# Kernel tuning notes

Measured on AMD Instinct MI355X. Metric: run time of the kernel, lower is better.

## Reference

```python
import jax, jax.numpy as jnp
import numpy as np

N_SRC = 100000
N_DST = 50000
N_EDGES = 1600000
D_IN = 128
D_OUT = 64


def setup_inputs() -> dict:
    key = jax.random.key(0)
    ks = jax.random.split(key, 6)
    x = jax.random.normal(ks[0], (N_SRC, D_IN), dtype=jnp.float32)
    W_l = jax.random.normal(ks[1], (D_IN, D_OUT), dtype=jnp.float32) * (1.0 / np.sqrt(D_IN))
    b_l = jax.random.normal(ks[2], (D_OUT,), dtype=jnp.float32) * 0.01
    W_r = jax.random.normal(ks[3], (D_IN, D_OUT), dtype=jnp.float32) * (1.0 / np.sqrt(D_IN))
    src = jax.random.randint(ks[4], (N_EDGES,), 0, N_SRC, dtype=jnp.int64)
    dst = jax.random.randint(ks[5], (N_EDGES,), 0, N_DST, dtype=jnp.int64)
    edge_index = jnp.stack([src, dst], axis=0)
    return {"x": x, "W_l": W_l, "b_l": b_l, "W_r": W_r,
            "edge_index": edge_index, "n_dst": N_DST}


def reference(x, W_l, b_l, W_r, edge_index, n_dst):
    src, dst = edge_index[0], edge_index[1]
    # gather source features along edges: [E, D_in]
    msgs = x[src]
    # mean aggregation at destination nodes
    agg = jax.ops.segment_sum(msgs, dst, num_segments=n_dst)          # [n_dst, D_in]
    cnt = jax.ops.segment_sum(jnp.ones_like(dst, dtype=x.dtype), dst,
                              num_segments=n_dst)                     # [n_dst]
    mean = agg / jnp.maximum(cnt, 1.0)[:, None]
    x_target = x[:n_dst]
    # SAGEConv: lin_l(mean_agg) + lin_r(x_target)
    out = mean @ W_l + b_l + x_target @ W_r                           # [n_dst, D_out]
    return jax.nn.log_softmax(out, axis=-1)
```

## Files before the change

### kernel.cpp

```cpp
#include <hip/hip_runtime.h>
#include <math.h>

#define DIN  128
#define DOUT 64
#define SLOT 96

__device__ inline unsigned short f2bf(float f) {
    unsigned u = __float_as_uint(f);
    u += 0x7fffu + ((u >> 16) & 1u);
    return (unsigned short)(u >> 16);
}
__device__ inline float bflo(unsigned u) { return __uint_as_float(u << 16); }
__device__ inline float bfhi(unsigned u) { return __uint_as_float(u & 0xffff0000u); }

__global__ void __launch_bounds__(256) build_k(
    const int* __restrict__ ei, unsigned* __restrict__ cnt,
    int* __restrict__ slots,
    const float* __restrict__ x, const float* __restrict__ Wl,
    const float* __restrict__ bl, const float* __restrict__ Wr,
    unsigned short* __restrict__ y, float* __restrict__ zout,
    int E, int nFill, int P, int nyb, int n_src, int n_dst, int cstr)
{
    __shared__ float s_x[16][DIN];
    const int b = blockIdx.x;
    const int fq = b / P;
    const bool isFill = ((b % P) == 0) && (fq < nFill);

    if (isFill) {
        int t = fq * 256 + threadIdx.x;
        int base = t * 8;
        if (base >= E) return;
        if (base + 8 <= E) {
            int4 sa = *(const int4*)(ei + base);
            int4 sb4 = *(const int4*)(ei + base + 4);
            int4 da = *(const int4*)(ei + E + base);
            int4 db = *(const int4*)(ei + E + base + 4);
            unsigned p0 = atomicAdd(&cnt[(size_t)da.x * cstr], 1u);
            unsigned p1 = atomicAdd(&cnt[(size_t)da.y * cstr], 1u);
            unsigned p2 = atomicAdd(&cnt[(size_t)da.z * cstr], 1u);
            unsigned p3 = atomicAdd(&cnt[(size_t)da.w * cstr], 1u);
            unsigned p4 = atomicAdd(&cnt[(size_t)db.x * cstr], 1u);
            unsigned p5 = atomicAdd(&cnt[(size_t)db.y * cstr], 1u);
            unsigned p6 = atomicAdd(&cnt[(size_t)db.z * cstr], 1u);
            unsigned p7 = atomicAdd(&cnt[(size_t)db.w * cstr], 1u);
            if (p0 < SLOT) slots[(size_t)da.x * SLOT + p0] = sa.x;
            if (p1 < SLOT) slots[(size_t)da.y * SLOT + p1] = sa.y;
            if (p2 < SLOT) slots[(size_t)da.z * SLOT + p2] = sa.z;
            if (p3 < SLOT) slots[(size_t)da.w * SLOT + p3] = sa.w;
            if (p4 < SLOT) slots[(size_t)db.x * SLOT + p4] = sb4.x;
            if (p5 < SLOT) slots[(size_t)db.y * SLOT + p5] = sb4.y;
            if (p6 < SLOT) slots[(size_t)db.z * SLOT + p6] = sb4.z;
            if (p7 < SLOT) slots[(size_t)db.w * SLOT + p7] = sb4.w;
        } else {
            for (int i = base; i < E && i < base + 8; ++i) {
                int s = ei[i], d = ei[E + i];
                unsigned p = atomicAdd(&cnt[(size_t)d * cstr], 1u);
                if (p < SLOT) slots[(size_t)d * SLOT + p] = s;
            }
        }
        return;
    }

    const int fillsBefore = (fq + 1 < nFill) ? (fq + 1) : nFill;
    const int pb   = b - fillsBefore;
    const int wave = threadIdx.x >> 6, lane = threadIdx.x & 63;
    const int sb = wave * 4;
    const bool isY = (pb < nyb);
    const int rowBase = (isY ? pb : pb - nyb) * 16 + sb;
    const int nRows = isY ? n_src : n_dst;
    const float* W = isY ? Wl : Wr;

    for (int r = 0; r < 4; ++r) {
        int row = rowBase + r;
        if (row >= nRows) continue;
        float2 v = *(const float2*)(x + (size_t)row * DIN + lane * 2);
        s_x[sb + r][lane * 2]     = v.x;
        s_x[sb + r][lane * 2 + 1] = v.y;
    }
    __syncthreads();

    float a0 = 0.f, a1 = 0.f, a2 = 0.f, a3 = 0.f;
    #pragma unroll 4
    for (int k = 0; k < DIN; ++k) {
        float w = W[k * DOUT + lane];
        a0 += s_x[sb + 0][k] * w;
        a1 += s_x[sb + 1][k] * w;
        a2 += s_x[sb + 2][k] * w;
        a3 += s_x[sb + 3][k] * w;
    }
    float acc[4] = {a0, a1, a2, a3};
    if (isY) {
        for (int r = 0; r < 4; ++r) {
            int row = rowBase + r;
            if (row < nRows) y[(size_t)row * DOUT + lane] = f2bf(acc[r]);
        }
    } else {
        const float bias = bl[lane];
        for (int r = 0; r < 4; ++r) {
            int row = rowBase + r;
            if (row < nRows) zout[(size_t)row * DOUT + lane] = acc[r] + bias;
        }
    }
}

__global__ void __launch_bounds__(256) gather_k(
    const unsigned short* __restrict__ y,
    const unsigned* __restrict__ cnt, const int* __restrict__ slots,
    float* __restrict__ out, int n_dst, int cstr)
{
    const int wave = threadIdx.x >> 6, lane = threadIdx.x & 63;
    const int row = blockIdx.x * 4 + wave;
    if (row >= n_dst) return;

    int deg = (int)cnt[(size_t)row * cstr];
    if (deg > SLOT) deg = SLOT;
    const int g = lane >> 4;
    const int qi = (lane & 15) * 2;
    const int q  = (lane & 15) * 4;
    const unsigned* yw = (const unsigned*)y;

    float4 ac0 = make_float4(0.f,0.f,0.f,0.f);
    float4 ac1 = make_float4(0.f,0.f,0.f,0.f);
    float4 ac2 = make_float4(0.f,0.f,0.f,0.f);
    float4 ac3 = make_float4(0.f,0.f,0.f,0.f);
    const int* srow = slots + (size_t)row * SLOT;

    for (int co = 0; co < deg; co += 64) {
        int rem = deg - co; if (rem > 64) rem = 64;
        int idx = (lane < rem) ? srow[co + lane] : 0;
        for (int i = 0; i < rem; i += 16) {
            int e0 = i + g, e1 = i + 4 + g, e2 = i + 8 + g, e3 = i + 12 + g;
            int s0 = __shfl(idx, e0), s1 = __shfl(idx, e1);
            int s2 = __shfl(idx, e2), s3 = __shfl(idx, e3);
            if (e0 < rem) { uint2 u = *(const uint2*)(yw + (size_t)s0 * 32 + qi);
                ac0.x += bflo(u.x); ac0.y += bfhi(u.x);
                ac0.z += bflo(u.y); ac0.w += bfhi(u.y); }
            if (e1 < rem) { uint2 u = *(const uint2*)(yw + (size_t)s1 * 32 + qi);
                ac1.x += bflo(u.x); ac1.y += bfhi(u.x);
                ac1.z += bflo(u.y); ac1.w += bfhi(u.y); }
            if (e2 < rem) { uint2 u = *(const uint2*)(yw + (size_t)s2 * 32 + qi);
                ac2.x += bflo(u.x); ac2.y += bfhi(u.x);
                ac2.z += bflo(u.y); ac2.w += bfhi(u.y); }
            if (e3 < rem) { uint2 u = *(const uint2*)(yw + (size_t)s3 * 32 + qi);
                ac3.x += bflo(u.x); ac3.y += bfhi(u.x);
                ac3.z += bflo(u.y); ac3.w += bfhi(u.y); }
        }
    }
    float4 acc;
    acc.x = (ac0.x + ac1.x) + (ac2.x + ac3.x);
    acc.y = (ac0.y + ac1.y) + (ac2.y + ac3.y);
    acc.z = (ac0.z + ac1.z) + (ac2.z + ac3.z);
    acc.w = (ac0.w + ac1.w) + (ac2.w + ac3.w);

    acc.x += __shfl_xor(acc.x, 32); acc.y += __shfl_xor(acc.y, 32);
    acc.z += __shfl_xor(acc.z, 32); acc.w += __shfl_xor(acc.w, 32);
    acc.x += __shfl_xor(acc.x, 16); acc.y += __shfl_xor(acc.y, 16);
    acc.z += __shfl_xor(acc.z, 16); acc.w += __shfl_xor(acc.w, 16);

    const float scale = 1.0f / (float)(deg > 0 ? deg : 1);
    const float4 zv = *(const float4*)(out + (size_t)row * DOUT + q);
    float4 v;
    v.x = acc.x * scale + zv.x;
    v.y = acc.y * scale + zv.y;
    v.z = acc.z * scale + zv.z;
    v.w = acc.w * scale + zv.w;

    float m = fmaxf(fmaxf(v.x, v.y), fmaxf(v.z, v.w));
    for (int o = 8; o >= 1; o >>= 1) m = fmaxf(m, __shfl_xor(m, o));
    float s = expf(v.x - m) + expf(v.y - m) + expf(v.z - m) + expf(v.w - m);
    for (int o = 8; o >= 1; o >>= 1) s += __shfl_xor(s, o);
    const float lse = m + logf(s);

    if (lane < 16) {
        float4 o4;
        o4.x = v.x - lse; o4.y = v.y - lse; o4.z = v.z - lse; o4.w = v.w - lse;
        *(float4*)(out + (size_t)row * DOUT + q) = o4;
    }
}

extern "C" void kernel_launch(void* const* d_in, const int* in_sizes, int n_in,
                              void* d_out, int out_size, void* d_ws, size_t ws_size,
                              hipStream_t stream)
{
    const float* x  = (const float*)d_in[0];
    const float* Wl = (const float*)d_in[1];
    const float* bl = (const float*)d_in[2];
    const float* Wr = (const float*)d_in[3];
    const int*   ei = (const int*)d_in[4];

    const int E     = in_sizes[4] / 2;
    const int n_src = in_sizes[0] / DIN;
    const int n_dst = out_size / DOUT;

    int cstr = 16;
    size_t need16 = (size_t)n_dst * cstr * 4 + (size_t)n_dst * SLOT * 4
                  + (size_t)n_src * DOUT * 2;
    if (need16 > ws_size) cstr = 1;

    unsigned*       cnt   = (unsigned*)d_ws;
    int*            slots = (int*)(cnt + (size_t)n_dst * cstr);
    unsigned short* yb    = (unsigned short*)(slots + (size_t)n_dst * SLOT);

    hipMemsetAsync(cnt, 0, (size_t)n_dst * cstr * sizeof(unsigned), stream);

    int nFill = (E + 2047) / 2048;
    int nyb = (n_src + 15) / 16;
    int nzb = (n_dst + 15) / 16;
    int nProj = nyb + nzb;
    int total = nFill + nProj;
    int P = (total + nFill - 1) / nFill;

    build_k<<<total, 256, 0, stream>>>(
        ei, cnt, slots, x, Wl, bl, Wr, yb, (float*)d_out,
        E, nFill, P, nyb, n_src, n_dst, cstr);

    int gG = (n_dst + 3) / 4;
    gather_k<<<gG, 256, 0, stream>>>(yb, cnt, slots, (float*)d_out, n_dst, cstr);
}
```

Measured before the change: 243.0 us.

## Use bf16 MFMA for node projections with prepacked weight fragments

```diff
diff --git a/kernel.cpp b/kernel.cpp
--- a/kernel.cpp
+++ b/kernel.cpp
@@ -4,6 +4,9 @@
 #define DIN  128
 #define DOUT 64
 #define SLOT 96
+
+typedef __attribute__((ext_vector_type(8))) short  short8;
+typedef __attribute__((ext_vector_type(4))) float  floatx4;
 
 __device__ inline unsigned short f2bf(float f) {
     unsigned u = __float_as_uint(f);
@@ -13,15 +16,36 @@
 __device__ inline float bflo(unsigned u) { return __uint_as_float(u << 16); }
 __device__ inline float bfhi(unsigned u) { return __uint_as_float(u & 0xffff0000u); }
 
+__global__ void __launch_bounds__(256) pack_k(const float* __restrict__ Wl,
+    const float* __restrict__ Wr, uint4* __restrict__ wb)
+{
+    int t = blockIdx.x * 256 + threadIdx.x;
+    if (t >= 2048) return;
+    int lane = t & 63;
+    int nt   = (t >> 6) & 3;
+    int kt   = (t >> 8) & 3;
+    int mat  = t >> 10;
+    const float* W = mat ? Wr : Wl;
+    int n  = nt * 16 + (lane & 15);
+    int k0 = kt * 32 + (lane >> 4) * 8;
+    unsigned h[8];
+    #pragma unroll
+    for (int j = 0; j < 8; ++j) h[j] = f2bf(W[(k0 + j) * DOUT + n]);
+    uint4 v;
+    v.x = h[0] | (h[1] << 16);
+    v.y = h[2] | (h[3] << 16);
+    v.z = h[4] | (h[5] << 16);
+    v.w = h[6] | (h[7] << 16);
+    wb[t] = v;
+}
+
 __global__ void __launch_bounds__(256) build_k(
     const int* __restrict__ ei, unsigned* __restrict__ cnt,
-    int* __restrict__ slots,
-    const float* __restrict__ x, const float* __restrict__ Wl,
-    const float* __restrict__ bl, const float* __restrict__ Wr,
+    int* __restrict__ slots, const uint4* __restrict__ wb,
+    const float* __restrict__ x, const float* __restrict__ bl,
     unsigned short* __restrict__ y, float* __restrict__ zout,
     int E, int nFill, int P, int nyb, int n_src, int n_dst, int cstr)
 {
-    __shared__ float s_x[16][DIN];
     const int b = blockIdx.x;
     const int fq = b / P;
     const bool isFill = ((b % P) == 0) && (fq < nFill);
@@ -64,41 +88,59 @@
     const int fillsBefore = (fq + 1 < nFill) ? (fq + 1) : nFill;
     const int pb   = b - fillsBefore;
     const int wave = threadIdx.x >> 6, lane = threadIdx.x & 63;
-    const int sb = wave * 4;
     const bool isY = (pb < nyb);
-    const int rowBase = (isY ? pb : pb - nyb) * 16 + sb;
+    const int tileBase = (isY ? pb : pb - nyb) * 64 + wave * 16;
     const int nRows = isY ? n_src : n_dst;
-    const float* W = isY ? Wl : Wr;
-
-    for (int r = 0; r < 4; ++r) {
-        int row = rowBase + r;
-        if (row >= nRows) continue;
-        float2 v = *(const float2*)(x + (size_t)row * DIN + lane * 2);
-        s_x[sb + r][lane * 2]     = v.x;
-        s_x[sb + r][lane * 2 + 1] = v.y;
-    }
-    __syncthreads();
-
-    float a0 = 0.f, a1 = 0.f, a2 = 0.f, a3 = 0.f;
-    #pragma unroll 4
-    for (int k = 0; k < DIN; ++k) {
-        float w = W[k * DOUT + lane];
-        a0 += s_x[sb + 0][k] * w;
-        a1 += s_x[sb + 1][k] * w;
-        a2 += s_x[sb + 2][k] * w;
-        a3 += s_x[sb + 3][k] * w;
-    }
-    float acc[4] = {a0, a1, a2, a3};
+    const int q = lane >> 4, n = lane & 15;
+
+    const short8* wfr = (const short8*)(wb + (isY ? 0 : 1024));
+    short8 bf[4][4];
+    #pragma unroll
+    for (int kt = 0; kt < 4; ++kt)
+        #pragma unroll
+        for (int nt = 0; nt < 4; ++nt)
+            bf[kt][nt] = wfr[(kt * 4 + nt) * 64 + lane];
+
+    int arow = tileBase + n;
+    if (arow >= nRows) arow = nRows - 1;
+    const float* xr = x + (size_t)arow * DIN + q * 8;
+
+    floatx4 acc[4] = {{0.f,0.f,0.f,0.f},{0.f,0.f,0.f,0.f},
+                      {0.f,0.f,0.f,0.f},{0.f,0.f,0.f,0.f}};
+    #pragma unroll
+    for (int kt = 0; kt < 4; ++kt) {
+        float4 u0 = *(const float4*)(xr + kt * 32);
+        float4 u1 = *(const float4*)(xr + kt * 32 + 4);
+        short8 a;
+        a[0] = (short)f2bf(u0.x); a[1] = (short)f2bf(u0.y);
+        a[2] = (short)f2bf(u0.z); a[3] = (short)f2bf(u0.w);
+        a[4] = (short)f2bf(u1.x); a[5] = (short)f2bf(u1.y);
+        a[6] = (short)f2bf(u1.z); a[7] = (short)f2bf(u1.w);
+        acc[0] = __builtin_amdgcn_mfma_f32_16x16x32_bf16(a, bf[kt][0], acc[0], 0, 0, 0);
+        acc[1] = __builtin_amdgcn_mfma_f32_16x16x32_bf16(a, bf[kt][1], acc[1], 0, 0, 0);
+        acc[2] = __builtin_amdgcn_mfma_f32_16x16x32_bf16(a, bf[kt][2], acc[2], 0, 0, 0);
+        acc[3] = __builtin_amdgcn_mfma_f32_16x16x32_bf16(a, bf[kt][3], acc[3], 0, 0, 0);
+    }
+
     if (isY) {
-        for (int r = 0; r < 4; ++r) {
-            int row = rowBase + r;
-            if (row < nRows) y[(size_t)row * DOUT + lane] = f2bf(acc[r]);
-        }
+        #pragma unroll
+        for (int nt = 0; nt < 4; ++nt)
+            #pragma unroll
+            for (int r = 0; r < 4; ++r) {
+                int row = tileBase + q * 4 + r;
+                if (row < nRows)
+                    y[(size_t)row * DOUT + nt * 16 + n] = f2bf(acc[nt][r]);
+            }
     } else {
-        const float bias = bl[lane];
-        for (int r = 0; r < 4; ++r) {
-            int row = rowBase + r;
-            if (row < nRows) zout[(size_t)row * DOUT + lane] = acc[r] + bias;
+        #pragma unroll
+        for (int nt = 0; nt < 4; ++nt) {
+            const float bias = bl[nt * 16 + n];
+            #pragma unroll
+            for (int r = 0; r < 4; ++r) {
+                int row = tileBase + q * 4 + r;
+                if (row < nRows)
+                    zout[(size_t)row * DOUT + nt * 16 + n] = acc[nt][r] + bias;
+            }
         }
     }
 }
@@ -194,24 +236,25 @@
 
     int cstr = 16;
     size_t need16 = (size_t)n_dst * cstr * 4 + (size_t)n_dst * SLOT * 4
-                  + (size_t)n_src * DOUT * 2;
+                  + (size_t)n_src * DOUT * 2 + 2048 * 16;
     if (need16 > ws_size) cstr = 1;
 
     unsigned*       cnt   = (unsigned*)d_ws;
     int*            slots = (int*)(cnt + (size_t)n_dst * cstr);
     unsigned short* yb    = (unsigned short*)(slots + (size_t)n_dst * SLOT);
+    uint4*          wb    = (uint4*)(yb + (size_t)n_src * DOUT);
 
     hipMemsetAsync(cnt, 0, (size_t)n_dst * cstr * sizeof(unsigned), stream);
+    pack_k<<<8, 256, 0, stream>>>(Wl, Wr, wb);
 
     int nFill = (E + 2047) / 2048;
-    int nyb = (n_src + 15) / 16;
-    int nzb = (n_dst + 15) / 16;
-    int nProj = nyb + nzb;
-    int total = nFill + nProj;
+    int nyb = (n_src + 63) / 64;
+    int nzb = (n_dst + 63) / 64;
+    int total = nFill + nyb + nzb;
     int P = (total + nFill - 1) / nFill;
 
     build_k<<<total, 256, 0, stream>>>(
-        ei, cnt, slots, x, Wl, bl, Wr, yb, (float*)d_out,
+        ei, cnt, slots, wb, x, bl, yb, (float*)d_out,
         E, nFill, P, nyb, n_src, n_dst, cstr);
 
     int gG = (n_dst + 3) / 4;
```

After: 253.4 us. +4.3%, slower.
